# Performance work log

Measured on AMD Instinct MI355X. Metric: run time of the kernel, lower is better.

Reference implementation:

```python
import jax, jax.numpy as jnp
import numpy as np

EPS = 1e-6
HEADS = 4


def _gather(x, idx):
    # x: (b,n,...), idx: (b,n,k) -> (b,n,k,...)
    return jax.vmap(lambda xb, ib: xb[ib])(x, idx)


def _prenorm(f0, f1):
    # FiberNorm: layernorm on scalars, norm-based RMS normalization on vectors
    mu = jnp.mean(f0, -1, keepdims=True)
    var = jnp.var(f0, -1, keepdims=True)
    g0 = (f0 - mu) * jax.lax.rsqrt(var + EPS)
    n1 = jnp.sum(f1 * f1, -1)  # (b,n,d1) squared channel norms
    rms = jax.lax.rsqrt(jnp.mean(n1, -1, keepdims=True) + EPS)  # (b,n,1)
    g1 = f1 * rms[..., None]
    return g0, g1


def _forward(f0, f1, coords, nbr_idx, Wq0, Wq1, Wk00, Wk10, Wk01, Wk11, Wk11r,
             Wv00, Wv10, Wv01, Wv11, Wv11r, Rw1, Rb1, Rw20, Rw21, Wo0, Wo1,
             F0w1, F0w2, F1w1, F1w2):
    b, n, d0 = f0.shape
    d1 = f1.shape[2]
    k = nbr_idx.shape[-1]
    L = Wq0.shape[0]
    # equivariant basis ingredients: relative positions over neighbor graph
    rel = _gather(coords, nbr_idx) - coords[:, :, None, :]       # (b,n,k,3)
    dist = jnp.linalg.norm(rel, axis=-1, keepdims=True)          # (b,n,k,1)
    rhat = rel / (dist + EPS)                                    # (b,n,k,3)
    scale = 1.0 / np.sqrt(d0 // HEADS + 3 * (d1 // HEADS)).astype(np.float32)
    for l in range(L):
        # ---- attention block (prenorm -> TFN attention -> residual) ----
        g0, g1 = _prenorm(f0, f1)
        rh = jax.nn.gelu(dist @ Rw1[l] + Rb1[l])                 # radial MLP (b,n,k,rh)
        r0 = rh @ Rw20[l]                                        # (b,n,k,d0)
        r1 = rh @ Rw21[l]                                        # (b,n,k,d1)
        q0 = g0 @ Wq0[l]                                         # (b,n,d0)
        q1 = jnp.einsum('bncm,ce->bnem', g1, Wq1[l])             # (b,n,d1,3)
        h0 = _gather(g0, nbr_idx)                                # (b,n,k,d0)
        h1 = _gather(g1, nbr_idx)                                # (b,n,k,d1,3)
        dot1 = jnp.einsum('bnkcm,bnkm->bnkc', h1, rhat)          # deg1->deg0 basis contraction
        k0 = (h0 @ Wk00[l] + dot1 @ Wk10[l]) * r0
        v0 = (h0 @ Wv00[l] + dot1 @ Wv10[l]) * r0
        rh_e = rhat[:, :, :, None, :]                            # (b,n,k,1,3)
        k1 = (jnp.einsum('bnkc,ce->bnke', h0, Wk01[l])[..., None] * rh_e
              + jnp.einsum('bnkcm,ce->bnkem', h1, Wk11[l])
              + jnp.einsum('bnkc,ce->bnke', dot1, Wk11r[l])[..., None] * rh_e) * r1[..., None]
        v1 = (jnp.einsum('bnkc,ce->bnke', h0, Wv01[l])[..., None] * rh_e
              + jnp.einsum('bnkcm,ce->bnkem', h1, Wv11[l])
              + jnp.einsum('bnkc,ce->bnke', dot1, Wv11r[l])[..., None] * rh_e) * r1[..., None]
        # multi-head invariant attention logits over neighbors
        hq0 = q0.reshape(b, n, HEADS, -1)
        hk0 = k0.reshape(b, n, k, HEADS, -1)
        hq1 = q1.reshape(b, n, HEADS, -1, 3)
        hk1 = k1.reshape(b, n, k, HEADS, -1, 3)
        logits = (jnp.einsum('bnhc,bnkhc->bnkh', hq0, hk0)
                  + jnp.einsum('bnhcm,bnkhcm->bnkh', hq1, hk1)) * scale
        a = jax.nn.softmax(logits, axis=2)                       # over neighbors
        o0 = jnp.einsum('bnkh,bnkhc->bnhc', a, v0.reshape(b, n, k, HEADS, -1)).reshape(b, n, d0)
        o1 = jnp.einsum('bnkh,bnkhcm->bnhcm', a, v1.reshape(b, n, k, HEADS, -1, 3)).reshape(b, n, d1, 3)
        f0 = f0 + o0 @ Wo0[l]
        f1 = f1 + jnp.einsum('bncm,ce->bnem', o1, Wo1[l])
        # ---- feedforward residual block (prenorm -> fiber FF -> residual) ----
        g0, g1 = _prenorm(f0, f1)
        f0 = f0 + jax.nn.gelu(g0 @ F0w1[l]) @ F0w2[l]
        u1 = jnp.einsum('bncm,ce->bnem', g1, F1w1[l])            # (b,n,4*d1,3)
        gate = jax.nn.sigmoid(jnp.linalg.norm(u1, axis=-1))     # norm-gated equivariant nonlin
        u1 = u1 * gate[..., None]
        f1 = f1 + jnp.einsum('bnem,ef->bnfm', u1, F1w2[l])
    return jnp.concatenate([f0, f1.reshape(b, n, d1 * 3)], axis=-1)


def setup_inputs() -> dict:
    key = jax.random.key(0)
    ks = iter(jax.random.split(key, 40))
    b, n, k, d0, d1, L, rh = 2, 4096, 32, 64, 16, 2, 16
    def w(shape, fan):
        return jax.random.normal(next(ks), shape, jnp.float32) / np.sqrt(fan).astype(np.float32)
    inp = {
        'f0': jax.random.normal(next(ks), (b, n, d0), jnp.float32),
        'f1': jax.random.normal(next(ks), (b, n, d1, 3), jnp.float32),
        'coords': jax.random.normal(next(ks), (b, n, 3), jnp.float32),
        'nbr_idx': jax.random.randint(next(ks), (b, n, k), 0, n),
        'Wq0': w((L, d0, d0), d0), 'Wq1': w((L, d1, d1), d1),
        'Wk00': w((L, d0, d0), d0), 'Wk10': w((L, d1, d0), d1),
        'Wk01': w((L, d0, d1), d0), 'Wk11': w((L, d1, d1), d1), 'Wk11r': w((L, d1, d1), d1),
        'Wv00': w((L, d0, d0), d0), 'Wv10': w((L, d1, d0), d1),
        'Wv01': w((L, d0, d1), d0), 'Wv11': w((L, d1, d1), d1), 'Wv11r': w((L, d1, d1), d1),
        'Rw1': w((L, 1, rh), 1), 'Rb1': jnp.zeros((L, rh), jnp.float32),
        'Rw20': w((L, rh, d0), rh), 'Rw21': w((L, rh, d1), rh),
        'Wo0': w((L, d0, d0), d0), 'Wo1': w((L, d1, d1), d1),
        'F0w1': w((L, d0, 4 * d0), d0), 'F0w2': w((L, 4 * d0, d0), 4 * d0),
        'F1w1': w((L, d1, 4 * d1), d1), 'F1w2': w((L, 4 * d1, d1), 4 * d1),
    }
    return inp


def reference(f0, f1, coords, nbr_idx, Wq0, Wq1, Wk00, Wk10, Wk01, Wk11, Wk11r,
              Wv00, Wv10, Wv01, Wv11, Wv11r, Rw1, Rb1, Rw20, Rw21, Wo0, Wo1,
              F0w1, F0w2, F1w1, F1w2):
    return _forward(f0, f1, coords, nbr_idx, Wq0, Wq1, Wk00, Wk10, Wk01, Wk11,
                    Wk11r, Wv00, Wv10, Wv01, Wv11, Wv11r, Rw1, Rb1, Rw20, Rw21,
                    Wo0, Wo1, F0w1, F0w2, F1w1, F1w2)
```

## Files before the change

kernel.cpp:

```cpp
#include <hip/hip_runtime.h>
#include <math.h>

#define BB    2
#define NN    4096
#define KK    32
#define D0    64
#define D1    16
#define D13   48
#define RHD   16
#define NHEAD 4
#define NLAYER 2
#define EPS   1e-6f
#define SCALE 0.18898223650461363f
#define ETOT  (BB*NN*KK)
#define AST   136
#define ARST  40

typedef float  f32x4 __attribute__((ext_vector_type(4)));
typedef short  s16x8 __attribute__((ext_vector_type(8)));
#define MFMA16(a,b,c) __builtin_amdgcn_mfma_f32_16x16x32_bf16(a,b,c,0,0,0)

__device__ __forceinline__ unsigned short f2bf(float x) {
    union { float f; unsigned u; } v; v.f = x;
    unsigned r = v.u + 0x7fffu + ((v.u >> 16) & 1u);
    return (unsigned short)(r >> 16);
}
__device__ __forceinline__ float bf2f(unsigned short h) {
    union { unsigned u; float f; } v; v.u = ((unsigned)h) << 16;
    return v.f;
}
__device__ __forceinline__ void split_bf(float x, unsigned short* hi, unsigned short* lo) {
    unsigned short h = f2bf(x);
    *hi = h;
    *lo = f2bf(x - bf2f(h));
}

__device__ __forceinline__ f32x4 mm3(s16x8 ah, s16x8 al, s16x8 bh, s16x8 bl, f32x4 c) {
    c = MFMA16(ah, bh, c);
    c = MFMA16(ah, bl, c);
    c = MFMA16(al, bh, c);
    return c;
}

__device__ __forceinline__ float wred(float v) {
    #pragma unroll
    for (int o = 32; o > 0; o >>= 1) v += __shfl_xor(v, o, 64);
    return v;
}

__device__ __forceinline__ float gelu_t(float x) {
    float x3 = x * x * x;
    return 0.5f * x * (1.0f + tanhf(0.7978845608028654f * (x + 0.044715f * x3)));
}

__global__ void geom_kernel(const float* __restrict__ coords,
                            const int* __restrict__ nbr,
                            float* __restrict__ rhat,
                            float* __restrict__ dist) {
    int e = blockIdx.x * blockDim.x + threadIdx.x;
    if (e >= ETOT) return;
    int bn = e / KK;
    int bb = bn / NN;
    int j  = nbr[e];
    const float* cs = coords + (size_t)bn * 3;
    const float* cn = coords + ((size_t)bb * NN + j) * 3;
    float rx = cn[0] - cs[0], ry = cn[1] - cs[1], rz = cn[2] - cs[2];
    float d  = sqrtf(rx * rx + ry * ry + rz * rz);
    float iv = 1.0f / (d + EPS);
    rhat[e * 3 + 0] = rx * iv;
    rhat[e * 3 + 1] = ry * iv;
    rhat[e * 3 + 2] = rz * iv;
    dist[e] = d;
}

__global__ __launch_bounds__(64) void prenorm_q_kernel(
    const float* __restrict__ f0, const float* __restrict__ f1,
    const float* __restrict__ Wq0, const float* __restrict__ Wq1,
    float* __restrict__ g0, float* __restrict__ g1,
    float* __restrict__ q0, float* __restrict__ q1) {
    int node = blockIdx.x;
    int lane = threadIdx.x;
    __shared__ float g0s[D0], g1s[D13];

    float x  = f0[(size_t)node * D0 + lane];
    float mu = wred(x) * (1.0f / D0);
    float dv = x - mu;
    float var = wred(dv * dv) * (1.0f / D0);
    float g0v = dv * rsqrtf(var + EPS);
    g0[(size_t)node * D0 + lane] = g0v;
    g0s[lane] = g0v;

    float w = (lane < D13) ? f1[(size_t)node * D13 + lane] : 0.0f;
    float t = wred(w * w);
    float rms = rsqrtf(t * (1.0f / D1) + EPS);
    if (lane < D13) {
        float g1v = w * rms;
        g1[(size_t)node * D13 + lane] = g1v;
        g1s[lane] = g1v;
    }
    __syncthreads();

    float acc = 0.0f;
    #pragma unroll
    for (int c = 0; c < D0; c++) acc += g0s[c] * Wq0[c * D0 + lane];
    q0[(size_t)node * D0 + lane] = acc;
    if (lane < D13) {
        int e = lane / 3, m = lane % 3;
        float a1 = 0.0f;
        #pragma unroll
        for (int c = 0; c < D1; c++) a1 += g1s[c * 3 + m] * Wq1[c * D1 + e];
        q1[(size_t)node * D13 + lane] = a1;
    }
}

__device__ __forceinline__ float B1val(int n, int k,
    const float* Wk00, const float* Wk10, const float* Wv00, const float* Wv10) {
    int nn = n & 63;
    const float* W0 = (n < 64) ? Wk00 : Wv00;
    const float* W1 = (n < 64) ? Wk10 : Wv10;
    if (k < 64) return W0[k * D0 + nn];
    if (k < 80) return W1[(k - 64) * D0 + nn];
    return 0.0f;
}
__device__ __forceinline__ float B2val(int n, int k,
    const float* Wk01, const float* Wk11, const float* Wk11r,
    const float* Wv01, const float* Wv11, const float* Wv11r) {
    if (n < 16) {
        if (k < 64) return Wk01[k * D1 + n];
        if (k < 80) return Wk11r[(k - 64) * D1 + n];
        return 0.0f;
    }
    if (n < 32) {
        int e = n - 16;
        if (k < 64) return Wv01[k * D1 + e];
        if (k < 80) return Wv11r[(k - 64) * D1 + e];
        return 0.0f;
    }
    if (n < 80) {
        int m = (n - 32) >> 4, e = (n - 32) & 15;
        if (k >= 80) { int mm = (k - 80) >> 4, c = (k - 80) & 15; if (mm == m) return Wk11[c * D1 + e]; }
        return 0.0f;
    }
    { int m = (n - 80) >> 4, e = (n - 80) & 15;
      if (k >= 80) { int mm = (k - 80) >> 4, c = (k - 80) & 15; if (mm == m) return Wv11[c * D1 + e]; }
      return 0.0f; }
}

__global__ void prep_kernel(
    const float* __restrict__ Wk00, const float* __restrict__ Wk10,
    const float* __restrict__ Wk01, const float* __restrict__ Wk11,
    const float* __restrict__ Wk11r,
    const float* __restrict__ Wv00, const float* __restrict__ Wv10,
    const float* __restrict__ Wv01, const float* __restrict__ Wv11,
    const float* __restrict__ Wv11r,
    const float* __restrict__ Rw20, const float* __restrict__ Rw21,
    unsigned short* __restrict__ B1H, unsigned short* __restrict__ B1L,
    unsigned short* __restrict__ B2H, unsigned short* __restrict__ B2L,
    unsigned short* __restrict__ R0H, unsigned short* __restrict__ R0L,
    unsigned short* __restrict__ R1H, unsigned short* __restrict__ R1L) {
    int id = blockIdx.x * 256 + threadIdx.x;
    if (id < 1536) {
        int ks = id >> 9, rem = id & 511, nt = rem >> 6, lane = rem & 63;
        int li = lane & 15, quad = lane >> 4;
        #pragma unroll
        for (int t = 0; t < 8; t++) {
            float v = B1val(nt * 16 + li, ks * 32 + quad * 8 + t, Wk00, Wk10, Wv00, Wv10);
            split_bf(v, &B1H[id * 8 + t], &B1L[id * 8 + t]);
        }
    } else if (id < 3584) {
        int id2 = id - 1536;
        int ks = id2 >> 9, rem = id2 & 511, nt = rem >> 6, lane = rem & 63;
        int li = lane & 15, quad = lane >> 4;
        #pragma unroll
        for (int t = 0; t < 8; t++) {
            float v = B2val(nt * 16 + li, ks * 32 + quad * 8 + t,
                            Wk01, Wk11, Wk11r, Wv01, Wv11, Wv11r);
            split_bf(v, &B2H[id2 * 8 + t], &B2L[id2 * 8 + t]);
        }
    } else if (id < 3840) {
        int id2 = id - 3584;
        int nt = id2 >> 6, lane = id2 & 63;
        int li = lane & 15, quad = lane >> 4;
        #pragma unroll
        for (int t = 0; t < 8; t++) {
            int k = quad * 8 + t;
            float v = (k < 16) ? Rw20[k * D0 + nt * 16 + li] : 0.0f;
            split_bf(v, &R0H[id2 * 8 + t], &R0L[id2 * 8 + t]);
        }
    } else if (id < 3904) {
        int id2 = id - 3840;
        int li = id2 & 15, quad = id2 >> 4;
        #pragma unroll
        for (int t = 0; t < 8; t++) {
            int k = quad * 8 + t;
            float v = (k < 16) ? Rw21[k * D1 + li] : 0.0f;
            split_bf(v, &R1H[id2 * 8 + t], &R1L[id2 * 8 + t]);
        }
    }
}

__global__ __launch_bounds__(128) void attn_fused_kernel(
    const float* __restrict__ g0g, const float* __restrict__ g1g,
    const int* __restrict__ nbr_idx,
    const float* __restrict__ rhatg, const float* __restrict__ distg,
    const float* __restrict__ q0g, const float* __restrict__ q1g,
    const float* __restrict__ Rw1, const float* __restrict__ Rb1,
    const unsigned short* __restrict__ B1H, const unsigned short* __restrict__ B1L,
    const unsigned short* __restrict__ B2H, const unsigned short* __restrict__ B2L,
    const unsigned short* __restrict__ R0H, const unsigned short* __restrict__ R0L,
    const unsigned short* __restrict__ R1H, const unsigned short* __restrict__ R1L,
    const float* __restrict__ Wo0, const float* __restrict__ Wo1,
    float* __restrict__ f0b, float* __restrict__ f1b) {

    int B0    = blockIdx.x * 64;
    int node0 = blockIdx.x * 2;
    int bb    = node0 >> 12;
    int tid   = threadIdx.x;
    int lane  = tid & 63, w = tid >> 6;
    int li    = lane & 15, quad = lane >> 4;

    __shared__ unsigned short AsH[64][AST], AsL[64][AST];
    __shared__ unsigned short ArH[64][ARST], ArL[64][ARST];
    __shared__ float rhts[64 * 3];
    __shared__ float dsts[64];
    __shared__ float q0s[2 * D0];
    __shared__ float q1s[2 * D13];
    __shared__ int   idxs[64];
    __shared__ float lgs[64][4];
    __shared__ float v1s[64][48];
    __shared__ float o0s[2][D0];
    __shared__ float o1s[2][D13];

    if (tid < 64) {
        idxs[tid] = nbr_idx[B0 + tid];
        dsts[tid] = distg[B0 + tid];
        rhts[tid]       = rhatg[(size_t)B0 * 3 + tid];
        rhts[tid + 64]  = rhatg[(size_t)B0 * 3 + tid + 64];
        rhts[tid + 128] = rhatg[(size_t)B0 * 3 + tid + 128];
    }
    q0s[tid] = q0g[(size_t)node0 * D0 + tid];
    if (tid < 96) q1s[tid] = q1g[(size_t)node0 * D13 + tid];
    __syncthreads();

    #pragma unroll
    for (int it = 0; it < 4; it++) {
        int v = tid + it * 128;
        int j = v >> 3, c8 = (v & 7) * 8;
        const float* src = g0g + ((size_t)bb * NN + idxs[j]) * D0 + c8;
        float4 x = *(const float4*)src;
        float4 y = *(const float4*)(src + 4);
        split_bf(x.x, &AsH[j][c8 + 0], &AsL[j][c8 + 0]);
        split_bf(x.y, &AsH[j][c8 + 1], &AsL[j][c8 + 1]);
        split_bf(x.z, &AsH[j][c8 + 2], &AsL[j][c8 + 2]);
        split_bf(x.w, &AsH[j][c8 + 3], &AsL[j][c8 + 3]);
        split_bf(y.x, &AsH[j][c8 + 4], &AsL[j][c8 + 4]);
        split_bf(y.y, &AsH[j][c8 + 5], &AsL[j][c8 + 5]);
        split_bf(y.z, &AsH[j][c8 + 6], &AsL[j][c8 + 6]);
        split_bf(y.w, &AsH[j][c8 + 7], &AsL[j][c8 + 7]);
    }
    #pragma unroll
    for (int it = 0; it < 8; it++) {
        int v = tid + it * 128;
        int j = v >> 4, c = v & 15;
        const float* src = g1g + ((size_t)bb * NN + idxs[j]) * D13 + c * 3;
        float a = src[0], b = src[1], cc = src[2];
        float d = a * rhts[j * 3] + b * rhts[j * 3 + 1] + cc * rhts[j * 3 + 2];
        split_bf(d,  &AsH[j][64 + c],  &AsL[j][64 + c]);
        split_bf(a,  &AsH[j][80 + c],  &AsL[j][80 + c]);
        split_bf(b,  &AsH[j][96 + c],  &AsL[j][96 + c]);
        split_bf(cc, &AsH[j][112 + c], &AsL[j][112 + c]);
    }
    #pragma unroll
    for (int it = 0; it < 8; it++) {
        int v = tid + it * 128;
        int j = v >> 4, u = v & 15;
        float x = gelu_t(dsts[j] * Rw1[u] + Rb1[u]);
        split_bf(x, &ArH[j][u], &ArL[j][u]);
        ArH[j][16 + u] = 0; ArL[j][16 + u] = 0;
    }
    __syncthreads();

    int mrow0 = w * 32 + li;
    int koff  = quad * 8;

    f32x4 r0a[2][4], r1a[2];
    #pragma unroll
    for (int i = 0; i < 2; i++) {
        #pragma unroll
        for (int j = 0; j < 4; j++) r0a[i][j] = (f32x4){0.f, 0.f, 0.f, 0.f};
        r1a[i] = (f32x4){0.f, 0.f, 0.f, 0.f};
    }
    {
        s16x8 rah0 = *(const s16x8*)&ArH[mrow0][koff];
        s16x8 ral0 = *(const s16x8*)&ArL[mrow0][koff];
        s16x8 rah1 = *(const s16x8*)&ArH[mrow0 + 16][koff];
        s16x8 ral1 = *(const s16x8*)&ArL[mrow0 + 16][koff];
        #pragma unroll
        for (int nt = 0; nt < 4; nt++) {
            s16x8 bh = *(const s16x8*)(R0H + (nt * 64 + lane) * 8);
            s16x8 bl = *(const s16x8*)(R0L + (nt * 64 + lane) * 8);
            r0a[0][nt] = mm3(rah0, ral0, bh, bl, r0a[0][nt]);
            r0a[1][nt] = mm3(rah1, ral1, bh, bl, r0a[1][nt]);
        }
        s16x8 bh = *(const s16x8*)(R1H + lane * 8);
        s16x8 bl = *(const s16x8*)(R1L + lane * 8);
        r1a[0] = mm3(rah0, ral0, bh, bl, r1a[0]);
        r1a[1] = mm3(rah1, ral1, bh, bl, r1a[1]);
    }

    f32x4 acc[2][8];
    #pragma unroll
    for (int i = 0; i < 2; i++)
        #pragma unroll
        for (int j = 0; j < 8; j++) acc[i][j] = (f32x4){0.f, 0.f, 0.f, 0.f};
    #pragma unroll
    for (int ks = 0; ks < 4; ks++) {
        int k0 = ks * 32 + koff;
        s16x8 ah0 = *(const s16x8*)&AsH[mrow0][k0];
        s16x8 al0 = *(const s16x8*)&AsL[mrow0][k0];
        s16x8 ah1 = *(const s16x8*)&AsH[mrow0 + 16][k0];
        s16x8 al1 = *(const s16x8*)&AsL[mrow0 + 16][k0];
        #pragma unroll
        for (int nt = 0; nt < 8; nt++) {
            s16x8 bh = *(const s16x8*)(B2H + ((ks * 8 + nt) * 64 + lane) * 8);
            s16x8 bl = *(const s16x8*)(B2L + ((ks * 8 + nt) * 64 + lane) * 8);
            acc[0][nt] = mm3(ah0, al0, bh, bl, acc[0][nt]);
            acc[1][nt] = mm3(ah1, al1, bh, bl, acc[1][nt]);
        }
    }

    #pragma unroll
    for (int mt = 0; mt < 2; mt++) {
        #pragma unroll
        for (int r = 0; r < 4; r++) {
            int j = w * 32 + mt * 16 + quad * 4 + r;
            float r1  = r1a[mt][r];
            float rh0 = rhts[j * 3], rh1 = rhts[j * 3 + 1], rh2 = rhts[j * 3 + 2];
            float sk = acc[mt][0][r], sv = acc[mt][1][r];
            float k1a = (sk * rh0 + acc[mt][2][r]) * r1;
            float k1b = (sk * rh1 + acc[mt][3][r]) * r1;
            float k1c = (sk * rh2 + acc[mt][4][r]) * r1;
            v1s[j][li * 3 + 0] = (sv * rh0 + acc[mt][5][r]) * r1;
            v1s[j][li * 3 + 1] = (sv * rh1 + acc[mt][6][r]) * r1;
            v1s[j][li * 3 + 2] = (sv * rh2 + acc[mt][7][r]) * r1;
            int qb = w * D13 + li * 3;
            float lc = q1s[qb] * k1a + q1s[qb + 1] * k1b + q1s[qb + 2] * k1c;
            lc += __shfl_xor(lc, 1, 4);
            lc += __shfl_xor(lc, 2, 4);
            if ((li & 3) == 0) lgs[j][li >> 2] = lc;
        }
    }
    __syncthreads();

    #pragma unroll
    for (int i = 0; i < 2; i++)
        #pragma unroll
        for (int j = 0; j < 8; j++) acc[i][j] = (f32x4){0.f, 0.f, 0.f, 0.f};
    #pragma unroll
    for (int ks = 0; ks < 3; ks++) {
        int k0 = ks * 32 + koff;
        s16x8 ah0 = *(const s16x8*)&AsH[mrow0][k0];
        s16x8 al0 = *(const s16x8*)&AsL[mrow0][k0];
        s16x8 ah1 = *(const s16x8*)&AsH[mrow0 + 16][k0];
        s16x8 al1 = *(const s16x8*)&AsL[mrow0 + 16][k0];
        #pragma unroll
        for (int nt = 0; nt < 8; nt++) {
            s16x8 bh = *(const s16x8*)(B1H + ((ks * 8 + nt) * 64 + lane) * 8);
            s16x8 bl = *(const s16x8*)(B1L + ((ks * 8 + nt) * 64 + lane) * 8);
            acc[0][nt] = mm3(ah0, al0, bh, bl, acc[0][nt]);
            acc[1][nt] = mm3(ah1, al1, bh, bl, acc[1][nt]);
        }
    }

    #pragma unroll
    for (int mt = 0; mt < 2; mt++) {
        int jb = w * 32 + mt * 16 + quad * 4;
        #pragma unroll
        for (int nt = 0; nt < 4; nt++) {
            float q0e = q0s[w * D0 + nt * 16 + li];
            float p[4];
            #pragma unroll
            for (int r = 0; r < 4; r++)
                p[r] = q0e * (acc[mt][nt][r] * r0a[mt][nt][r]);
            #pragma unroll
            for (int off = 1; off < 16; off <<= 1) {
                #pragma unroll
                for (int r = 0; r < 4; r++) p[r] += __shfl_xor(p[r], off, 16);
            }
            if (li == 0) {
                #pragma unroll
                for (int r = 0; r < 4; r++) lgs[jb + r][nt] += p[r];
            }
        }
    }
    __syncthreads();

    if (lane < NHEAD) {
        int h = lane;
        float mx = -1e30f;
        for (int jn = 0; jn < KK; jn++) mx = fmaxf(mx, lgs[w * 32 + jn][h]);
        float mxs = mx * SCALE;
        float s = 0.0f;
        for (int jn = 0; jn < KK; jn++) {
            float ex = expf(lgs[w * 32 + jn][h] * SCALE - mxs);
            lgs[w * 32 + jn][h] = ex;
            s += ex;
        }
        float iv = 1.0f / s;
        for (int jn = 0; jn < KK; jn++) lgs[w * 32 + jn][h] *= iv;
    }
    __syncthreads();

    #pragma unroll
    for (int nt = 0; nt < 4; nt++) {
        float p = 0.0f;
        #pragma unroll
        for (int mt = 0; mt < 2; mt++)
            #pragma unroll
            for (int r = 0; r < 4; r++) {
                int j = w * 32 + mt * 16 + quad * 4 + r;
                p += lgs[j][nt] * (acc[mt][nt + 4][r] * r0a[mt][nt][r]);
            }
        p += __shfl_xor(p, 16, 64);
        p += __shfl_xor(p, 32, 64);
        if (quad == 0) o0s[w][nt * 16 + li] = p;
    }
    if (lane < D13) {
        int h = (lane / 3) >> 2;
        float p = 0.0f;
        #pragma unroll
        for (int jn = 0; jn < KK; jn++)
            p += lgs[w * 32 + jn][h] * v1s[w * 32 + jn][lane];
        o1s[w][lane] = p;
    }
    __syncthreads();

    {
        float a0 = 0.0f;
        #pragma unroll
        for (int e = 0; e < D0; e++) a0 += o0s[w][e] * Wo0[e * D0 + lane];
        f0b[(size_t)(node0 + w) * D0 + lane] += a0;
    }
    if (lane < D13) {
        int f = lane / 3, m = lane % 3;
        float a1 = 0.0f;
        #pragma unroll
        for (int c = 0; c < D1; c++) a1 += o1s[w][c * 3 + m] * Wo1[c * D1 + f];
        f1b[(size_t)(node0 + w) * D13 + lane] += a1;
    }
}

__global__ __launch_bounds__(256) void ffn_kernel(
    const float* __restrict__ F0w1, const float* __restrict__ F0w2,
    const float* __restrict__ F1w1, const float* __restrict__ F1w2,
    float* __restrict__ f0b, float* __restrict__ f1b) {
    int node = blockIdx.x;
    int tid  = threadIdx.x;
    __shared__ float g0s[D0], g1s[D13], ts[256], us[D13 * 4];

    if (tid < 64) {
        float x  = f0b[(size_t)node * D0 + tid];
        float mu = wred(x) * (1.0f / D0);
        float dv = x - mu;
        float var = wred(dv * dv) * (1.0f / D0);
        g0s[tid] = dv * rsqrtf(var + EPS);
    } else if (tid < 128) {
        int lane = tid - 64;
        float ww = (lane < D13) ? f1b[(size_t)node * D13 + lane] : 0.0f;
        float t = wred(ww * ww);
        float rms = rsqrtf(t * (1.0f / D1) + EPS);
        if (lane < D13) g1s[lane] = ww * rms;
    }
    __syncthreads();

    {
        float acc = 0.0f;
        #pragma unroll
        for (int c = 0; c < D0; c++) acc += g0s[c] * F0w1[c * 256 + tid];
        ts[tid] = gelu_t(acc);
    }
    if (tid < 192) {
        int e = tid / 3, m = tid % 3;
        float acc = 0.0f;
        #pragma unroll
        for (int c = 0; c < D1; c++) acc += g1s[c * 3 + m] * F1w1[c * 64 + e];
        us[tid] = acc;
    }
    __syncthreads();

    if (tid < 64) {
        int e = tid;
        float a = us[e * 3], b = us[e * 3 + 1], c = us[e * 3 + 2];
        float nrm = sqrtf(a * a + b * b + c * c);
        float gate = 1.0f / (1.0f + expf(-nrm));
        us[e * 3 + 0] *= gate;
        us[e * 3 + 1] *= gate;
        us[e * 3 + 2] *= gate;
    }
    __syncthreads();

    if (tid < 64) {
        float acc = 0.0f;
        #pragma unroll
        for (int j = 0; j < 256; j++) acc += ts[j] * F0w2[j * D0 + tid];
        f0b[(size_t)node * D0 + tid] += acc;
    } else if (tid < 112) {
        int idx = tid - 64, f = idx / 3, m = idx % 3;
        float acc = 0.0f;
        #pragma unroll
        for (int e = 0; e < 64; e++) acc += us[e * 3 + m] * F1w2[e * D1 + f];
        f1b[(size_t)node * D13 + idx] += acc;
    }
}

__global__ void concat_kernel(const float* __restrict__ f0b,
                              const float* __restrict__ f1b,
                              float* __restrict__ out) {
    int i = blockIdx.x * blockDim.x + threadIdx.x;
    if (i >= BB * NN * (D0 + D13)) return;
    int node = i / (D0 + D13), c = i % (D0 + D13);
    out[i] = (c < D0) ? f0b[(size_t)node * D0 + c]
                      : f1b[(size_t)node * D13 + (c - D0)];
}

extern "C" void kernel_launch(void* const* d_in, const int* in_sizes, int n_in,
                              void* d_out, int out_size, void* d_ws, size_t ws_size,
                              hipStream_t stream) {
    const float* f0     = (const float*)d_in[0];
    const float* f1     = (const float*)d_in[1];
    const float* coords = (const float*)d_in[2];
    const int*   nbr    = (const int*)d_in[3];
    const float* Wq0    = (const float*)d_in[4];
    const float* Wq1    = (const float*)d_in[5];
    const float* Wk00   = (const float*)d_in[6];
    const float* Wk10   = (const float*)d_in[7];
    const float* Wk01   = (const float*)d_in[8];
    const float* Wk11   = (const float*)d_in[9];
    const float* Wk11r  = (const float*)d_in[10];
    const float* Wv00   = (const float*)d_in[11];
    const float* Wv10   = (const float*)d_in[12];
    const float* Wv01   = (const float*)d_in[13];
    const float* Wv11   = (const float*)d_in[14];
    const float* Wv11r  = (const float*)d_in[15];
    const float* Rw1    = (const float*)d_in[16];
    const float* Rb1    = (const float*)d_in[17];
    const float* Rw20   = (const float*)d_in[18];
    const float* Rw21   = (const float*)d_in[19];
    const float* Wo0    = (const float*)d_in[20];
    const float* Wo1    = (const float*)d_in[21];
    const float* F0w1   = (const float*)d_in[22];
    const float* F0w2   = (const float*)d_in[23];
    const float* F1w1   = (const float*)d_in[24];
    const float* F1w2   = (const float*)d_in[25];
    float* out = (float*)d_out;

    int nodes = BB * NN;

    float* wf = (float*)d_ws;
    float* f0b   = wf; wf += (size_t)nodes * D0;
    float* f1b   = wf; wf += (size_t)nodes * D13;
    float* g0b   = wf; wf += (size_t)nodes * D0;
    float* g1b   = wf; wf += (size_t)nodes * D13;
    float* q0b   = wf; wf += (size_t)nodes * D0;
    float* q1b   = wf; wf += (size_t)nodes * D13;
    float* rhatb = wf; wf += (size_t)ETOT * 3;
    float* distb = wf; wf += (size_t)ETOT;
    unsigned short* wu = (unsigned short*)wf;
    unsigned short* B1H = wu; wu += 1536 * 8;
    unsigned short* B1L = wu; wu += 1536 * 8;
    unsigned short* B2H = wu; wu += 2048 * 8;
    unsigned short* B2L = wu; wu += 2048 * 8;
    unsigned short* R0H = wu; wu += 256 * 8;
    unsigned short* R0L = wu; wu += 256 * 8;
    unsigned short* R1H = wu; wu += 64 * 8;
    unsigned short* R1L = wu; wu += 64 * 8;

    geom_kernel<<<(ETOT + 255) / 256, 256, 0, stream>>>(coords, nbr, rhatb, distb);
    hipMemcpyAsync(f0b, f0, (size_t)nodes * D0 * sizeof(float),
                   hipMemcpyDeviceToDevice, stream);
    hipMemcpyAsync(f1b, f1, (size_t)nodes * D13 * sizeof(float),
                   hipMemcpyDeviceToDevice, stream);

    for (int l = 0; l < NLAYER; l++) {
        prenorm_q_kernel<<<nodes, 64, 0, stream>>>(
            f0b, f1b, Wq0 + l * D0 * D0, Wq1 + l * D1 * D1, g0b, g1b, q0b, q1b);
        prep_kernel<<<16, 256, 0, stream>>>(
            Wk00 + l * D0 * D0, Wk10 + l * D1 * D0,
            Wk01 + l * D0 * D1, Wk11 + l * D1 * D1, Wk11r + l * D1 * D1,
            Wv00 + l * D0 * D0, Wv10 + l * D1 * D0,
            Wv01 + l * D0 * D1, Wv11 + l * D1 * D1, Wv11r + l * D1 * D1,
            Rw20 + l * RHD * D0, Rw21 + l * RHD * D1,
            B1H, B1L, B2H, B2L, R0H, R0L, R1H, R1L);
        attn_fused_kernel<<<ETOT / 64, 128, 0, stream>>>(
            g0b, g1b, nbr, rhatb, distb, q0b, q1b,
            Rw1 + l * RHD, Rb1 + l * RHD,
            B1H, B1L, B2H, B2L, R0H, R0L, R1H, R1L,
            Wo0 + l * D0 * D0, Wo1 + l * D1 * D1,
            f0b, f1b);
        ffn_kernel<<<nodes, 256, 0, stream>>>(
            F0w1 + l * D0 * 256, F0w2 + l * 256 * D0,
            F1w1 + l * D1 * 64, F1w2 + l * 64 * D1,
            f0b, f1b);
    }

    concat_kernel<<<(nodes * (D0 + D13) + 255) / 256, 256, 0, stream>>>(f0b, f1b, out);
}
```

Baseline: 545.6 us.

## Precompute bf16 split operands in global memory and feed MFMA directly from gathers

```diff
diff --git a/kernel.cpp b/kernel.cpp
--- a/kernel.cpp
+++ b/kernel.cpp
@@ -13,8 +13,6 @@
 #define EPS   1e-6f
 #define SCALE 0.18898223650461363f
 #define ETOT  (BB*NN*KK)
-#define AST   136
-#define ARST  40
 
 typedef float  f32x4 __attribute__((ext_vector_type(4)));
 typedef short  s16x8 __attribute__((ext_vector_type(8)));
@@ -76,8 +74,10 @@
 __global__ __launch_bounds__(64) void prenorm_q_kernel(
     const float* __restrict__ f0, const float* __restrict__ f1,
     const float* __restrict__ Wq0, const float* __restrict__ Wq1,
-    float* __restrict__ g0, float* __restrict__ g1,
-    float* __restrict__ q0, float* __restrict__ q1) {
+    float* __restrict__ g1,
+    float* __restrict__ q0, float* __restrict__ q1,
+    unsigned short* __restrict__ g0H, unsigned short* __restrict__ g0L,
+    unsigned short* __restrict__ g1mH, unsigned short* __restrict__ g1mL) {
     int node = blockIdx.x;
     int lane = threadIdx.x;
     __shared__ float g0s[D0], g1s[D13];
@@ -87,7 +87,7 @@
     float dv = x - mu;
     float var = wred(dv * dv) * (1.0f / D0);
     float g0v = dv * rsqrtf(var + EPS);
-    g0[(size_t)node * D0 + lane] = g0v;
+    split_bf(g0v, &g0H[(size_t)node * D0 + lane], &g0L[(size_t)node * D0 + lane]);
     g0s[lane] = g0v;
 
     float w = (lane < D13) ? f1[(size_t)node * D13 + lane] : 0.0f;
@@ -97,6 +97,9 @@
         float g1v = w * rms;
         g1[(size_t)node * D13 + lane] = g1v;
         g1s[lane] = g1v;
+        int c = lane / 3, m = lane % 3;
+        split_bf(g1v, &g1mH[(size_t)node * D13 + m * 16 + c],
+                      &g1mL[(size_t)node * D13 + m * 16 + c]);
     }
     __syncthreads();
 
@@ -111,6 +114,25 @@
         for (int c = 0; c < D1; c++) a1 += g1s[c * 3 + m] * Wq1[c * D1 + e];
         q1[(size_t)node * D13 + lane] = a1;
     }
+}
+
+__global__ __launch_bounds__(256) void edge_prep_kernel(
+    const int* __restrict__ nbr,
+    const float* __restrict__ rhatb, const float* __restrict__ distb,
+    const float* __restrict__ g1b,
+    const float* __restrict__ Rw1, const float* __restrict__ Rb1,
+    unsigned short* __restrict__ d1H, unsigned short* __restrict__ d1L,
+    unsigned short* __restrict__ rhHg, unsigned short* __restrict__ rhLg) {
+    int t = blockIdx.x * 256 + threadIdx.x;
+    int e = t >> 4, c = t & 15;
+    int bn = e >> 5;
+    int bb = bn >> 12;
+    int nj = nbr[e];
+    const float* g1 = g1b + ((size_t)bb * NN + nj) * D13 + c * 3;
+    float d1 = g1[0] * rhatb[e * 3] + g1[1] * rhatb[e * 3 + 1] + g1[2] * rhatb[e * 3 + 2];
+    split_bf(d1, &d1H[t], &d1L[t]);
+    float rh = gelu_t(distb[e] * Rw1[c] + Rb1[c]);
+    split_bf(rh, &rhHg[t], &rhLg[t]);
 }
 
 __device__ __forceinline__ float B1val(int n, int k,
@@ -200,11 +222,13 @@
 }
 
 __global__ __launch_bounds__(128) void attn_fused_kernel(
-    const float* __restrict__ g0g, const float* __restrict__ g1g,
     const int* __restrict__ nbr_idx,
-    const float* __restrict__ rhatg, const float* __restrict__ distg,
+    const float* __restrict__ rhatg,
     const float* __restrict__ q0g, const float* __restrict__ q1g,
-    const float* __restrict__ Rw1, const float* __restrict__ Rb1,
+    const unsigned short* __restrict__ g0H, const unsigned short* __restrict__ g0L,
+    const unsigned short* __restrict__ g1mH, const unsigned short* __restrict__ g1mL,
+    const unsigned short* __restrict__ d1H, const unsigned short* __restrict__ d1L,
+    const unsigned short* __restrict__ rhHg, const unsigned short* __restrict__ rhLg,
     const unsigned short* __restrict__ B1H, const unsigned short* __restrict__ B1L,
     const unsigned short* __restrict__ B2H, const unsigned short* __restrict__ B2L,
     const unsigned short* __restrict__ R0H, const unsigned short* __restrict__ R0L,
@@ -219,69 +243,25 @@
     int lane  = tid & 63, w = tid >> 6;
     int li    = lane & 15, quad = lane >> 4;
 
-    __shared__ unsigned short AsH[64][AST], AsL[64][AST];
-    __shared__ unsigned short ArH[64][ARST], ArL[64][ARST];
-    __shared__ float rhts[64 * 3];
-    __shared__ float dsts[64];
-    __shared__ float q0s[2 * D0];
-    __shared__ float q1s[2 * D13];
-    __shared__ int   idxs[64];
+    __shared__ float rhts[2][96];
     __shared__ float lgs[64][4];
-    __shared__ float v1s[64][48];
+    __shared__ float v1s[64][49];
     __shared__ float o0s[2][D0];
     __shared__ float o1s[2][D13];
 
-    if (tid < 64) {
-        idxs[tid] = nbr_idx[B0 + tid];
-        dsts[tid] = distg[B0 + tid];
-        rhts[tid]       = rhatg[(size_t)B0 * 3 + tid];
-        rhts[tid + 64]  = rhatg[(size_t)B0 * 3 + tid + 64];
-        rhts[tid + 128] = rhatg[(size_t)B0 * 3 + tid + 128];
-    }
-    q0s[tid] = q0g[(size_t)node0 * D0 + tid];
-    if (tid < 96) q1s[tid] = q1g[(size_t)node0 * D13 + tid];
-    __syncthreads();
-
-    #pragma unroll
-    for (int it = 0; it < 4; it++) {
-        int v = tid + it * 128;
-        int j = v >> 3, c8 = (v & 7) * 8;
-        const float* src = g0g + ((size_t)bb * NN + idxs[j]) * D0 + c8;
-        float4 x = *(const float4*)src;
-        float4 y = *(const float4*)(src + 4);
-        split_bf(x.x, &AsH[j][c8 + 0], &AsL[j][c8 + 0]);
-        split_bf(x.y, &AsH[j][c8 + 1], &AsL[j][c8 + 1]);
-        split_bf(x.z, &AsH[j][c8 + 2], &AsL[j][c8 + 2]);
-        split_bf(x.w, &AsH[j][c8 + 3], &AsL[j][c8 + 3]);
-        split_bf(y.x, &AsH[j][c8 + 4], &AsL[j][c8 + 4]);
-        split_bf(y.y, &AsH[j][c8 + 5], &AsL[j][c8 + 5]);
-        split_bf(y.z, &AsH[j][c8 + 6], &AsL[j][c8 + 6]);
-        split_bf(y.w, &AsH[j][c8 + 7], &AsL[j][c8 + 7]);
-    }
-    #pragma unroll
-    for (int it = 0; it < 8; it++) {
-        int v = tid + it * 128;
-        int j = v >> 4, c = v & 15;
-        const float* src = g1g + ((size_t)bb * NN + idxs[j]) * D13 + c * 3;
-        float a = src[0], b = src[1], cc = src[2];
-        float d = a * rhts[j * 3] + b * rhts[j * 3 + 1] + cc * rhts[j * 3 + 2];
-        split_bf(d,  &AsH[j][64 + c],  &AsL[j][64 + c]);
-        split_bf(a,  &AsH[j][80 + c],  &AsL[j][80 + c]);
-        split_bf(b,  &AsH[j][96 + c],  &AsL[j][96 + c]);
-        split_bf(cc, &AsH[j][112 + c], &AsL[j][112 + c]);
-    }
-    #pragma unroll
-    for (int it = 0; it < 8; it++) {
-        int v = tid + it * 128;
-        int j = v >> 4, u = v & 15;
-        float x = gelu_t(dsts[j] * Rw1[u] + Rb1[u]);
-        split_bf(x, &ArH[j][u], &ArL[j][u]);
-        ArH[j][16 + u] = 0; ArL[j][16 + u] = 0;
-    }
-    __syncthreads();
-
-    int mrow0 = w * 32 + li;
-    int koff  = quad * 8;
+    if (lane < 32) {
+        int base = (B0 + w * 32) * 3;
+        rhts[w][lane]      = rhatg[base + lane];
+        rhts[w][lane + 32] = rhatg[base + lane + 32];
+        rhts[w][lane + 64] = rhatg[base + lane + 64];
+    }
+    __syncthreads();
+
+    size_t e0 = (size_t)B0 + w * 32 + li, e1 = e0 + 16;
+    size_t n0 = (size_t)bb * NN + nbr_idx[e0];
+    size_t n1 = (size_t)bb * NN + nbr_idx[e1];
+
+    int koff = quad * 8;
 
     f32x4 r0a[2][4], r1a[2];
     #pragma unroll
@@ -291,10 +271,14 @@
         r1a[i] = (f32x4){0.f, 0.f, 0.f, 0.f};
     }
     {
-        s16x8 rah0 = *(const s16x8*)&ArH[mrow0][koff];
-        s16x8 ral0 = *(const s16x8*)&ArL[mrow0][koff];
-        s16x8 rah1 = *(const s16x8*)&ArH[mrow0 + 16][koff];
-        s16x8 ral1 = *(const s16x8*)&ArL[mrow0 + 16][koff];
+        s16x8 zz = (s16x8){0,0,0,0,0,0,0,0};
+        s16x8 rah0 = zz, ral0 = zz, rah1 = zz, ral1 = zz;
+        if (quad < 2) {
+            rah0 = *(const s16x8*)(rhHg + e0 * 16 + koff);
+            ral0 = *(const s16x8*)(rhLg + e0 * 16 + koff);
+            rah1 = *(const s16x8*)(rhHg + e1 * 16 + koff);
+            ral1 = *(const s16x8*)(rhLg + e1 * 16 + koff);
+        }
         #pragma unroll
         for (int nt = 0; nt < 4; nt++) {
             s16x8 bh = *(const s16x8*)(R0H + (nt * 64 + lane) * 8);
@@ -308,6 +292,23 @@
         r1a[1] = mm3(rah1, ral1, bh, bl, r1a[1]);
     }
 
+    #define APTRS(ks, nb, ee, PH, PL)                                              \
+        const unsigned short *PH, *PL;                                             \
+        if (ks < 2) {                                                              \
+            PH = g0H + (nb) * 64 + ks * 32 + koff;                                 \
+            PL = g0L + (nb) * 64 + ks * 32 + koff;                                 \
+        } else if (ks == 2) {                                                      \
+            PH = (quad < 2) ? d1H + (ee) * 16 + quad * 8                           \
+                            : g1mH + (nb) * 48 + (quad - 2) * 8;                   \
+            PL = (quad < 2) ? d1L + (ee) * 16 + quad * 8                           \
+                            : g1mL + (nb) * 48 + (quad - 2) * 8;                   \
+        } else {                                                                   \
+            PH = (quad < 2) ? g1mH + (nb) * 48 + 16 + quad * 8                     \
+                            : g1mH + (nb) * 48 + 32 + (quad - 2) * 8;              \
+            PL = (quad < 2) ? g1mL + (nb) * 48 + 16 + quad * 8                     \
+                            : g1mL + (nb) * 48 + 32 + (quad - 2) * 8;              \
+        }
+
     f32x4 acc[2][8];
     #pragma unroll
     for (int i = 0; i < 2; i++)
@@ -315,11 +316,10 @@
         for (int j = 0; j < 8; j++) acc[i][j] = (f32x4){0.f, 0.f, 0.f, 0.f};
     #pragma unroll
     for (int ks = 0; ks < 4; ks++) {
-        int k0 = ks * 32 + koff;
-        s16x8 ah0 = *(const s16x8*)&AsH[mrow0][k0];
-        s16x8 al0 = *(const s16x8*)&AsL[mrow0][k0];
-        s16x8 ah1 = *(const s16x8*)&AsH[mrow0 + 16][k0];
-        s16x8 al1 = *(const s16x8*)&AsL[mrow0 + 16][k0];
+        APTRS(ks, n0, e0, pH0, pL0)
+        APTRS(ks, n1, e1, pH1, pL1)
+        s16x8 ah0 = *(const s16x8*)pH0, al0 = *(const s16x8*)pL0;
+        s16x8 ah1 = *(const s16x8*)pH1, al1 = *(const s16x8*)pL1;
         #pragma unroll
         for (int nt = 0; nt < 8; nt++) {
             s16x8 bh = *(const s16x8*)(B2H + ((ks * 8 + nt) * 64 + lane) * 8);
@@ -329,25 +329,30 @@
         }
     }
 
-    #pragma unroll
-    for (int mt = 0; mt < 2; mt++) {
-        #pragma unroll
-        for (int r = 0; r < 4; r++) {
-            int j = w * 32 + mt * 16 + quad * 4 + r;
-            float r1  = r1a[mt][r];
-            float rh0 = rhts[j * 3], rh1 = rhts[j * 3 + 1], rh2 = rhts[j * 3 + 2];
-            float sk = acc[mt][0][r], sv = acc[mt][1][r];
-            float k1a = (sk * rh0 + acc[mt][2][r]) * r1;
-            float k1b = (sk * rh1 + acc[mt][3][r]) * r1;
-            float k1c = (sk * rh2 + acc[mt][4][r]) * r1;
-            v1s[j][li * 3 + 0] = (sv * rh0 + acc[mt][5][r]) * r1;
-            v1s[j][li * 3 + 1] = (sv * rh1 + acc[mt][6][r]) * r1;
-            v1s[j][li * 3 + 2] = (sv * rh2 + acc[mt][7][r]) * r1;
-            int qb = w * D13 + li * 3;
-            float lc = q1s[qb] * k1a + q1s[qb + 1] * k1b + q1s[qb + 2] * k1c;
-            lc += __shfl_xor(lc, 1, 4);
-            lc += __shfl_xor(lc, 2, 4);
-            if ((li & 3) == 0) lgs[j][li >> 2] = lc;
+    {
+        float q1v0 = q1g[(size_t)(node0 + w) * D13 + li * 3 + 0];
+        float q1v1 = q1g[(size_t)(node0 + w) * D13 + li * 3 + 1];
+        float q1v2 = q1g[(size_t)(node0 + w) * D13 + li * 3 + 2];
+        #pragma unroll
+        for (int mt = 0; mt < 2; mt++) {
+            #pragma unroll
+            for (int r = 0; r < 4; r++) {
+                int jl = mt * 16 + quad * 4 + r;
+                int jj = w * 32 + jl;
+                float r1  = r1a[mt][r];
+                float rh0 = rhts[w][jl * 3], rh1 = rhts[w][jl * 3 + 1], rh2 = rhts[w][jl * 3 + 2];
+                float sk = acc[mt][0][r], sv = acc[mt][1][r];
+                float k1a = (sk * rh0 + acc[mt][2][r]) * r1;
+                float k1b = (sk * rh1 + acc[mt][3][r]) * r1;
+                float k1c = (sk * rh2 + acc[mt][4][r]) * r1;
+                v1s[jj][li * 3 + 0] = (sv * rh0 + acc[mt][5][r]) * r1;
+                v1s[jj][li * 3 + 1] = (sv * rh1 + acc[mt][6][r]) * r1;
+                v1s[jj][li * 3 + 2] = (sv * rh2 + acc[mt][7][r]) * r1;
+                float lc = q1v0 * k1a + q1v1 * k1b + q1v2 * k1c;
+                lc += __shfl_xor(lc, 1, 4);
+                lc += __shfl_xor(lc, 2, 4);
+                if ((li & 3) == 0) lgs[jj][li >> 2] = lc;
+            }
         }
     }
     __syncthreads();
@@ -358,11 +363,10 @@
         for (int j = 0; j < 8; j++) acc[i][j] = (f32x4){0.f, 0.f, 0.f, 0.f};
     #pragma unroll
     for (int ks = 0; ks < 3; ks++) {
-        int k0 = ks * 32 + koff;
-        s16x8 ah0 = *(const s16x8*)&AsH[mrow0][k0];
-        s16x8 al0 = *(const s16x8*)&AsL[mrow0][k0];
-        s16x8 ah1 = *(const s16x8*)&AsH[mrow0 + 16][k0];
-        s16x8 al1 = *(const s16x8*)&AsL[mrow0 + 16][k0];
+        APTRS(ks, n0, e0, pH0, pL0)
+        APTRS(ks, n1, e1, pH1, pL1)
+        s16x8 ah0 = *(const s16x8*)pH0, al0 = *(const s16x8*)pL0;
+        s16x8 ah1 = *(const s16x8*)pH1, al1 = *(const s16x8*)pL1;
         #pragma unroll
         for (int nt = 0; nt < 8; nt++) {
             s16x8 bh = *(const s16x8*)(B1H + ((ks * 8 + nt) * 64 + lane) * 8);
@@ -372,24 +376,29 @@
         }
     }
 
-    #pragma unroll
-    for (int mt = 0; mt < 2; mt++) {
-        int jb = w * 32 + mt * 16 + quad * 4;
-        #pragma unroll
-        for (int nt = 0; nt < 4; nt++) {
-            float q0e = q0s[w * D0 + nt * 16 + li];
-            float p[4];
+    {
+        float q0e[4];
+        #pragma unroll
+        for (int nt = 0; nt < 4; nt++)
+            q0e[nt] = q0g[(size_t)(node0 + w) * D0 + nt * 16 + li];
+        #pragma unroll
+        for (int mt = 0; mt < 2; mt++) {
+            int jb = w * 32 + mt * 16 + quad * 4;
             #pragma unroll
-            for (int r = 0; r < 4; r++)
-                p[r] = q0e * (acc[mt][nt][r] * r0a[mt][nt][r]);
-            #pragma unroll
-            for (int off = 1; off < 16; off <<= 1) {
+            for (int nt = 0; nt < 4; nt++) {
+                float p[4];
                 #pragma unroll
-                for (int r = 0; r < 4; r++) p[r] += __shfl_xor(p[r], off, 16);
-            }
-            if (li == 0) {
+                for (int r = 0; r < 4; r++)
+                    p[r] = q0e[nt] * (acc[mt][nt][r] * r0a[mt][nt][r]);
                 #pragma unroll
-                for (int r = 0; r < 4; r++) lgs[jb + r][nt] += p[r];
+                for (int off = 1; off < 16; off <<= 1) {
+                    #pragma unroll
+                    for (int r = 0; r < 4; r++) p[r] += __shfl_xor(p[r], off, 16);
+                }
+                if (li == 0) {
+                    #pragma unroll
+                    for (int r = 0; r < 4; r++) lgs[jb + r][nt] += p[r];
+                }
             }
         }
     }
@@ -448,6 +457,7 @@
         for (int c = 0; c < D1; c++) a1 += o1s[w][c * 3 + m] * Wo1[c * D1 + f];
         f1b[(size_t)(node0 + w) * D13 + lane] += a1;
     }
+    #undef APTRS
 }
 
 __global__ __launch_bounds__(256) void ffn_kernel(
@@ -559,13 +569,20 @@
     float* wf = (float*)d_ws;
     float* f0b   = wf; wf += (size_t)nodes * D0;
     float* f1b   = wf; wf += (size_t)nodes * D13;
-    float* g0b   = wf; wf += (size_t)nodes * D0;
     float* g1b   = wf; wf += (size_t)nodes * D13;
     float* q0b   = wf; wf += (size_t)nodes * D0;
     float* q1b   = wf; wf += (size_t)nodes * D13;
     float* rhatb = wf; wf += (size_t)ETOT * 3;
     float* distb = wf; wf += (size_t)ETOT;
     unsigned short* wu = (unsigned short*)wf;
+    unsigned short* g0H  = wu; wu += (size_t)nodes * D0;
+    unsigned short* g0L  = wu; wu += (size_t)nodes * D0;
+    unsigned short* g1mH = wu; wu += (size_t)nodes * D13;
+    unsigned short* g1mL = wu; wu += (size_t)nodes * D13;
+    unsigned short* d1H  = wu; wu += (size_t)ETOT * 16;
+    unsigned short* d1L  = wu; wu += (size_t)ETOT * 16;
+    unsigned short* rhH  = wu; wu += (size_t)ETOT * 16;
+    unsigned short* rhL  = wu; wu += (size_t)ETOT * 16;
     unsigned short* B1H = wu; wu += 1536 * 8;
     unsigned short* B1L = wu; wu += 1536 * 8;
     unsigned short* B2H = wu; wu += 2048 * 8;
@@ -583,7 +600,8 @@
 
     for (int l = 0; l < NLAYER; l++) {
         prenorm_q_kernel<<<nodes, 64, 0, stream>>>(
-            f0b, f1b, Wq0 + l * D0 * D0, Wq1 + l * D1 * D1, g0b, g1b, q0b, q1b);
+            f0b, f1b, Wq0 + l * D0 * D0, Wq1 + l * D1 * D1,
+            g1b, q0b, q1b, g0H, g0L, g1mH, g1mL);
         prep_kernel<<<16, 256, 0, stream>>>(
             Wk00 + l * D0 * D0, Wk10 + l * D1 * D0,
             Wk01 + l * D0 * D1, Wk11 + l * D1 * D1, Wk11r + l * D1 * D1,
@@ -591,9 +609,12 @@
             Wv01 + l * D0 * D1, Wv11 + l * D1 * D1, Wv11r + l * D1 * D1,
             Rw20 + l * RHD * D0, Rw21 + l * RHD * D1,
             B1H, B1L, B2H, B2L, R0H, R0L, R1H, R1L);
+        edge_prep_kernel<<<ETOT * 16 / 256, 256, 0, stream>>>(
+            nbr, rhatb, distb, g1b, Rw1 + l * RHD, Rb1 + l * RHD,
+            d1H, d1L, rhH, rhL);
         attn_fused_kernel<<<ETOT / 64, 128, 0, stream>>>(
-            g0b, g1b, nbr, rhatb, distb, q0b, q1b,
-            Rw1 + l * RHD, Rb1 + l * RHD,
+            nbr, rhatb, q0b, q1b,
+            g0H, g0L, g1mH, g1mL, d1H, d1L, rhH, rhL,
             B1H, B1L, B2H, B2L, R0H, R0L, R1H, R1L,
             Wo0 + l * D0 * D0, Wo1 + l * D1 * D1,
             f0b, f1b);
```

Result: slower. 567.3 us (+4.0%).
